# Kernel tuning notes

Measured on AMD Instinct MI355X. Metric: run time of the kernel, lower is better.

Reference implementation:

```python
import jax, jax.numpy as jnp
import numpy as np

B, N, ENC, DEC, E, ATT, V, T = 64, 196, 2048, 512, 512, 512, 32000, 32


def setup_inputs() -> dict:
    key = jax.random.key(0)
    ks = jax.random.split(key, 12)
    s = 0.02  # param init scale
    f = lambda k, shape: jax.random.normal(k, shape, jnp.float32) * s
    return {
        "features": jax.random.normal(ks[0], (B, N, ENC), jnp.float32),
        "captions": jax.random.randint(ks[1], (B, T), 0, V),
        "emb": f(ks[2], (V, E)),
        "att_Wenc": f(ks[3], (ENC, ATT)),
        "att_Wdec": f(ks[4], (DEC, ATT)),
        "att_v": f(ks[5], (ATT,)),
        "init_h_W": f(ks[6], (ENC, DEC)), "init_h_b": jnp.zeros((DEC,), jnp.float32),
        "init_c_W": f(ks[7], (ENC, DEC)), "init_c_b": jnp.zeros((DEC,), jnp.float32),
        "W_ih": f(ks[8], (4 * DEC, E + ENC)), "W_hh": f(ks[9], (4 * DEC, DEC)),
        "b_ih": jnp.zeros((4 * DEC,), jnp.float32), "b_hh": jnp.zeros((4 * DEC,), jnp.float32),
        "out_W": f(ks[10], (DEC, V)), "out_b": jnp.zeros((V,), jnp.float32),
    }


def reference(features, captions, emb, att_Wenc, att_Wdec, att_v,
              init_h_W, init_h_b, init_c_W, init_c_b,
              W_ih, W_hh, b_ih, b_hh, out_W, out_b):
    # init hidden/cell from mean-pooled encoder features
    mean_f = features.mean(axis=1)                      # [B, ENC]
    h = mean_f @ init_h_W + init_h_b                    # [B, DEC]
    c = mean_f @ init_c_W + init_c_b                    # [B, DEC]

    enc_att = features @ att_Wenc                       # [B, N, ATT] (loop-invariant)
    embs = emb[captions]                                # [B, T, E]
    xs = jnp.swapaxes(embs[:, :-1], 0, 1)               # [T-1, B, E] time-major

    def step(carry, x):
        h, c = carry
        # Bahdanau attention: tanh(Wf + Wh) . v -> softmax over spatial locations
        e = jnp.tanh(enc_att + (h @ att_Wdec)[:, None, :]) @ att_v   # [B, N]
        alpha = jax.nn.softmax(e, axis=1)                            # [B, N]
        context = jnp.einsum('bn,bnd->bd', alpha, features)          # [B, ENC]
        lstm_in = jnp.concatenate([x, context], axis=1)              # [B, E+ENC]
        gates = lstm_in @ W_ih.T + b_ih + h @ W_hh.T + b_hh          # [B, 4*DEC]
        i, f, g, o = jnp.split(gates, 4, axis=1)                     # torch gate order
        c = jax.nn.sigmoid(f) * c + jax.nn.sigmoid(i) * jnp.tanh(g)
        h = jax.nn.sigmoid(o) * jnp.tanh(c)
        out = h @ out_W + out_b                                      # dropout = identity (eval)
        return (h, c), (out, alpha)

    _, (preds, alphas) = jax.lax.scan(step, (h, c), xs)
    # back to batch-major: preds [B, T-1, V], alphas [B, T-1, N]
    return jnp.swapaxes(preds, 0, 1), jnp.swapaxes(alphas, 0, 1)
```

## Files before the change

kernel.cpp:

```cpp
#include <hip/hip_runtime.h>
#include <math.h>

constexpr int kB = 64, kN = 196, kENC = 2048, kDEC = 512, kE = 512, kATT = 512;
constexpr int kV = 32000, kT = 32, kTS = 31;
constexpr int kKIH = kE + kENC;
constexpr int kKG  = kENC + kDEC;
constexpr int kG   = 4 * kDEC;
constexpr int kSPL = 8, kKSP = kKG / kSPL;
constexpr int kM   = kTS * kB;
constexpr int kMP  = 2048;

typedef __attribute__((ext_vector_type(8))) short bf8;
typedef __attribute__((ext_vector_type(4))) float f4;
typedef __attribute__((ext_vector_type(4))) unsigned u4;

__device__ __forceinline__ f4 mfma16(bf8 a, bf8 b, f4 c){
  asm("v_mfma_f32_16x16x32_bf16 %0, %1, %2, %0" : "+v"(c) : "v"(a), "v"(b));
  return c;
}
__device__ __forceinline__ float bf2f(unsigned short u){
  return __uint_as_float(((unsigned)u) << 16);
}
__device__ __forceinline__ unsigned short f2b(float f){
  unsigned u = __float_as_uint(f);
  u += 0x7fffu + ((u >> 16) & 1u);
  return (unsigned short)(u >> 16);
}
__device__ __forceinline__ float th_(float x){
  float e2 = __expf(2.f * x);
  return 1.f - 2.f * __builtin_amdgcn_rcpf(e2 + 1.f);
}
__device__ __forceinline__ float sg_(float x){
  return __builtin_amdgcn_rcpf(1.f + __expf(-x));
}

__global__ void k_cvt(const float* __restrict__ src, unsigned short* __restrict__ dst, int n8){
  int i = blockIdx.x * 256 + threadIdx.x;
  if (i >= n8) return;
  float4 a = ((const float4*)src)[2 * i];
  float4 b = ((const float4*)src)[2 * i + 1];
  union { unsigned short u[8]; uint4 v; } t;
  t.u[0] = f2b(a.x); t.u[1] = f2b(a.y); t.u[2] = f2b(a.z); t.u[3] = f2b(a.w);
  t.u[4] = f2b(b.x); t.u[5] = f2b(b.y); t.u[6] = f2b(b.z); t.u[7] = f2b(b.w);
  ((uint4*)dst)[i] = t.v;
}

__global__ __launch_bounds__(256) void k_tcvt(const float* __restrict__ src,
                                              unsigned short* __restrict__ dst, int R, int C){
  __shared__ float t[32][33];
  int c0 = blockIdx.x * 32, r0 = blockIdx.y * 32;
  int tx = threadIdx.x & 31, ty = threadIdx.x >> 5;
  #pragma unroll
  for (int j = 0; j < 4; j++)
    t[ty + 8*j][tx] = src[(size_t)(r0 + ty + 8*j) * C + c0 + tx];
  __syncthreads();
  #pragma unroll
  for (int j = 0; j < 4; j++)
    dst[(size_t)(c0 + ty + 8*j) * R + r0 + tx] = f2b(t[tx][ty + 8*j]);
}

__global__ __launch_bounds__(256) void k_tf32(const float* __restrict__ src,
                                              float* __restrict__ dst, int R, int C){
  __shared__ float t[32][33];
  int c0 = blockIdx.x * 32, r0 = blockIdx.y * 32;
  int tx = threadIdx.x & 31, ty = threadIdx.x >> 5;
  #pragma unroll
  for (int j = 0; j < 4; j++)
    t[ty + 8*j][tx] = src[(size_t)(r0 + ty + 8*j) * C + c0 + tx];
  __syncthreads();
  #pragma unroll
  for (int j = 0; j < 4; j++)
    dst[(size_t)(c0 + ty + 8*j) * R + r0 + tx] = t[tx][ty + 8*j];
}

__global__ void k_mean(const float* __restrict__ feat, float* __restrict__ meanf){
  int b = blockIdx.x, d = blockIdx.y * 256 + threadIdx.x;
  const float* p = feat + (size_t)b * kN * kENC + d;
  float s = 0.f;
  for (int n = 0; n < kN; n++) s += p[(size_t)n * kENC];
  meanf[b * kENC + d] = s * (1.f / kN);
}

__global__ __launch_bounds__(512) void k_init(const float* __restrict__ meanf,
                       const float* __restrict__ Wh, const float* __restrict__ bh,
                       const float* __restrict__ Wc, const float* __restrict__ bc,
                       float* __restrict__ h, float* __restrict__ c){
  __shared__ float mf[kENC];
  int b = blockIdx.x;
  for (int i = threadIdx.x; i < kENC; i += 512) mf[i] = meanf[b * kENC + i];
  __syncthreads();
  int j = threadIdx.x;
  const float* W  = blockIdx.y ? Wc : Wh;
  const float* bb = blockIdx.y ? bc : bh;
  float acc = bb[j];
  for (int k = 0; k < kENC; k++) acc = fmaf(mf[k], W[k * kDEC + j], acc);
  (blockIdx.y ? c : h)[b * kDEC + j] = acc;
}

__global__ __launch_bounds__(512) void k_gather(const float* __restrict__ emb,
        const int* __restrict__ captions, unsigned short* __restrict__ Xemb){
  int m = blockIdx.x;
  int t = m >> 6, b = m & 63, d = threadIdx.x;
  Xemb[(size_t)m * kE + d] = f2b(emb[(size_t)captions[b * kT + t] * kE + d]);
}

template<int K, int LDA, int LDB, int LDC>
__global__ __launch_bounds__(256) void k_gemm_nt(const unsigned short* __restrict__ A,
                                                 const unsigned short* __restrict__ Bt,
                                                 unsigned short* __restrict__ Cb){
  int w = threadIdx.x >> 6, lane = threadIdx.x & 63;
  int m0 = blockIdx.x * 64 + w * 16, n0 = blockIdx.y * 64;
  int lr = lane & 15, lk = (lane >> 4) * 8;
  f4 acc[4] = {};
  const unsigned short* Ap = A  + (size_t)(m0 + lr) * LDA + lk;
  const unsigned short* Bp = Bt + (size_t)(n0 + lr) * LDB + lk;
  #pragma unroll 4
  for (int k0 = 0; k0 < K; k0 += 32){
    bf8 a  = *(const bf8*)(Ap + k0);
    bf8 b0 = *(const bf8*)(Bp + k0);
    bf8 b1 = *(const bf8*)(Bp + (size_t)16 * LDB + k0);
    bf8 b2 = *(const bf8*)(Bp + (size_t)32 * LDB + k0);
    bf8 b3 = *(const bf8*)(Bp + (size_t)48 * LDB + k0);
    acc[0] = mfma16(a, b0, acc[0]); acc[1] = mfma16(a, b1, acc[1]);
    acc[2] = mfma16(a, b2, acc[2]); acc[3] = mfma16(a, b3, acc[3]);
  }
  asm volatile("s_nop 7\n\ts_nop 7");
  int orow = (lane >> 4) * 4;
  #pragma unroll
  for (int nt = 0; nt < 4; nt++)
    #pragma unroll
    for (int r = 0; r < 4; r++)
      Cb[(size_t)(m0 + orow + r) * LDC + n0 + nt*16 + lr] = f2b(acc[nt][r]);
}

__global__ __launch_bounds__(256) void k_e(const unsigned short* __restrict__ EA,
                   const float* __restrict__ hWdec,
                   const float* __restrict__ attv, float* __restrict__ e){
  int w = threadIdx.x >> 6, lane = threadIdx.x & 63;
  int r = blockIdx.x * 4 + w;
  int b = r / kN;
  u4 ev = *(const u4*)(EA + (size_t)r * kATT + lane * 8);
  const float* hp = hWdec + b * kATT + lane * 8;
  const float* ap = attv + lane * 8;
  float4 h0 = *(const float4*)hp, h1 = *(const float4*)(hp + 4);
  float4 v0 = *(const float4*)ap, v1 = *(const float4*)(ap + 4);
  float s = 0.f;
  s = fmaf(th_(bf2f((unsigned short)(ev.x & 0xffffu)) + h0.x), v0.x, s);
  s = fmaf(th_(bf2f((unsigned short)(ev.x >> 16))     + h0.y), v0.y, s);
  s = fmaf(th_(bf2f((unsigned short)(ev.y & 0xffffu)) + h0.z), v0.z, s);
  s = fmaf(th_(bf2f((unsigned short)(ev.y >> 16))     + h0.w), v0.w, s);
  s = fmaf(th_(bf2f((unsigned short)(ev.z & 0xffffu)) + h1.x), v1.x, s);
  s = fmaf(th_(bf2f((unsigned short)(ev.z >> 16))     + h1.y), v1.y, s);
  s = fmaf(th_(bf2f((unsigned short)(ev.w & 0xffffu)) + h1.z), v1.z, s);
  s = fmaf(th_(bf2f((unsigned short)(ev.w >> 16))     + h1.w), v1.w, s);
  #pragma unroll
  for (int off = 32; off; off >>= 1) s += __shfl_xor(s, off, 64);
  if (lane == 0) e[r] = s;
}

__global__ __launch_bounds__(256) void k_ctx(const float* __restrict__ e,
                     const unsigned short* __restrict__ featb,
                     unsigned short* __restrict__ Xb, float* __restrict__ alphas, int t){
  __shared__ float al[kN];
  __shared__ float red[256];
  __shared__ float cred[4][64][8];
  int b = blockIdx.x, q = blockIdx.y, tid = threadIdx.x;
  float ev = (tid < kN) ? e[b * kN + tid] : -1e30f;
  red[tid] = ev; __syncthreads();
  for (int off = 128; off; off >>= 1){ if (tid < off) red[tid] = fmaxf(red[tid], red[tid + off]); __syncthreads(); }
  float mx = red[0]; __syncthreads();
  float ex = (tid < kN) ? __expf(ev - mx) : 0.f;
  red[tid] = ex; __syncthreads();
  for (int off = 128; off; off >>= 1){ if (tid < off) red[tid] += red[tid + off]; __syncthreads(); }
  float inv = 1.f / red[0];
  if (tid < kN){
    float a = ex * inv;
    al[tid] = a;
    if (q == 0) alphas[((size_t)b * kTS + t) * kN + tid] = a;
  }
  __syncthreads();
  int g = tid & 63, nq = tid >> 6;
  int d0 = q * 512 + g * 8;
  const unsigned short* fp = featb + (size_t)b * kN * kENC + d0;
  float c[8] = {0.f,0.f,0.f,0.f,0.f,0.f,0.f,0.f};
  int nbeg = nq * 49, nend = nbeg + 49;
  #pragma unroll 7
  for (int n = nbeg; n < nend; ++n){
    u4 v = *(const u4*)(fp + (size_t)n * kENC);
    float a = al[n];
    c[0] = fmaf(bf2f((unsigned short)(v.x & 0xffffu)), a, c[0]);
    c[1] = fmaf(bf2f((unsigned short)(v.x >> 16)),     a, c[1]);
    c[2] = fmaf(bf2f((unsigned short)(v.y & 0xffffu)), a, c[2]);
    c[3] = fmaf(bf2f((unsigned short)(v.y >> 16)),     a, c[3]);
    c[4] = fmaf(bf2f((unsigned short)(v.z & 0xffffu)), a, c[4]);
    c[5] = fmaf(bf2f((unsigned short)(v.z >> 16)),     a, c[5]);
    c[6] = fmaf(bf2f((unsigned short)(v.w & 0xffffu)), a, c[6]);
    c[7] = fmaf(bf2f((unsigned short)(v.w >> 16)),     a, c[7]);
  }
  if (nq){
    #pragma unroll
    for (int j = 0; j < 8; j++) cred[nq][g][j] = c[j];
  }
  __syncthreads();
  if (nq == 0){
    unsigned outw[4];
    #pragma unroll
    for (int j = 0; j < 4; j++){
      float lo = c[2*j]   + cred[1][g][2*j]   + cred[2][g][2*j]   + cred[3][g][2*j];
      float hi = c[2*j+1] + cred[1][g][2*j+1] + cred[2][g][2*j+1] + cred[3][g][2*j+1];
      outw[j] = ((unsigned)f2b(hi) << 16) | (unsigned)f2b(lo);
    }
    *(u4*)(Xb + (size_t)b * kKG + d0) = *(u4*)outw;
  }
}

__global__ __launch_bounds__(256) void k_gates(const unsigned short* __restrict__ X,
        const unsigned short* __restrict__ Wih, const unsigned short* __restrict__ Whh,
        float* __restrict__ gpart){
  int w = threadIdx.x >> 6, lane = threadIdx.x & 63;
  int n0 = blockIdx.x * 64 + w * 16, ks = blockIdx.y;
  int lr = lane & 15, lk = (lane >> 4) * 8;
  int nrow = n0 + lr;
  f4 acc[4] = {};
  const unsigned short* Xp = X + (size_t)lr * kKG + ks * kKSP + lk;
  #pragma unroll 2
  for (int kt = 0; kt < kKSP; kt += 32){
    int kk = ks * kKSP + kt + lk;
    bf8 a0 = *(const bf8*)(Xp + kt);
    bf8 a1 = *(const bf8*)(Xp + 16 * kKG + kt);
    bf8 a2 = *(const bf8*)(Xp + 32 * kKG + kt);
    bf8 a3 = *(const bf8*)(Xp + 48 * kKG + kt);
    const unsigned short* bp = (kk < kENC) ? (Wih + (size_t)nrow * kKIH + kE + kk)
                                           : (Whh + (size_t)nrow * kDEC + (kk - kENC));
    bf8 b = *(const bf8*)bp;
    acc[0] = mfma16(a0, b, acc[0]); acc[1] = mfma16(a1, b, acc[1]);
    acc[2] = mfma16(a2, b, acc[2]); acc[3] = mfma16(a3, b, acc[3]);
  }
  asm volatile("s_nop 7\n\ts_nop 7");
  float* gp = gpart + (size_t)ks * kB * kG;
  int orow = (lane >> 4) * 4;
  #pragma unroll
  for (int mt = 0; mt < 4; mt++)
    #pragma unroll
    for (int r = 0; r < 4; r++)
      gp[(size_t)(mt*16 + orow + r) * kG + n0 + lr] = acc[mt][r];
}

__global__ __launch_bounds__(512) void k_lstm(const float* __restrict__ gpart,
      const unsigned short* __restrict__ Gxb,
      const float* __restrict__ bih, const float* __restrict__ bhh,
      float* __restrict__ c, unsigned short* __restrict__ Xb,
      unsigned short* __restrict__ Hall,
      const float* __restrict__ WdecT, float* __restrict__ hWdec, int t){
  __shared__ float hl[kDEC];
  int b = blockIdx.x, d = threadIdx.x;
  int m = t * kB + b;
  float gi = 0.f, gf = 0.f, gg = 0.f, go = 0.f;
  for (int ks = 0; ks < kSPL; ks++){
    const float* gp = gpart + ((size_t)ks * kB + b) * kG;
    gi += gp[d]; gf += gp[kDEC + d]; gg += gp[2*kDEC + d]; go += gp[3*kDEC + d];
  }
  const unsigned short* gx = Gxb + (size_t)m * kG;
  gi += bf2f(gx[d])          + bih[d]          + bhh[d];
  gf += bf2f(gx[kDEC + d])   + bih[kDEC + d]   + bhh[kDEC + d];
  gg += bf2f(gx[2*kDEC + d]) + bih[2*kDEC + d] + bhh[2*kDEC + d];
  go += bf2f(gx[3*kDEC + d]) + bih[3*kDEC + d] + bhh[3*kDEC + d];
  float cn = sg_(gf) * c[b*kDEC + d] + sg_(gi) * th_(gg);
  float hn = sg_(go) * th_(cn);
  c[b*kDEC + d] = cn;
  hl[d] = hn;
  unsigned short hb = f2b(hn);
  Xb[(size_t)b*kKG + kENC + d] = hb;
  Hall[((size_t)b*kTS + t)*kDEC + d] = hb;
  __syncthreads();
  const float* wr = WdecT + (size_t)d * kATT;
  float a = 0.f;
  #pragma unroll 8
  for (int kk = 0; kk < kATT; kk += 4){
    float4 wv = *(const float4*)(wr + kk);
    a = fmaf(wv.x, hl[kk + 0], a);
    a = fmaf(wv.y, hl[kk + 1], a);
    a = fmaf(wv.z, hl[kk + 2], a);
    a = fmaf(wv.w, hl[kk + 3], a);
  }
  hWdec[b * kATT + d] = a;
}

__global__ __launch_bounds__(512) void k_prep(const float* __restrict__ h0,
      unsigned short* __restrict__ Xb,
      const float* __restrict__ WdecT, float* __restrict__ hWdec){
  __shared__ float hl[kDEC];
  int b = blockIdx.x, d = threadIdx.x;
  float hv = h0[b*kDEC + d];
  hl[d] = hv;
  Xb[(size_t)b*kKG + kENC + d] = f2b(hv);
  __syncthreads();
  const float* wr = WdecT + (size_t)d * kATT;
  float a = 0.f;
  #pragma unroll 8
  for (int kk = 0; kk < kATT; kk += 4){
    float4 wv = *(const float4*)(wr + kk);
    a = fmaf(wv.x, hl[kk + 0], a);
    a = fmaf(wv.y, hl[kk + 1], a);
    a = fmaf(wv.z, hl[kk + 2], a);
    a = fmaf(wv.w, hl[kk + 3], a);
  }
  hWdec[b * kATT + d] = a;
}

__global__ __launch_bounds__(512) void k_bigout(const unsigned short* __restrict__ Hall,
        const unsigned short* __restrict__ Wt,
        const float* __restrict__ bias, float* __restrict__ preds){
  __shared__ float st[64][128];
  int w = threadIdx.x >> 6, lane = threadIdx.x & 63;
  int n0 = blockIdx.x * 128, m0 = blockIdx.y * 256;
  int lr = lane & 15, lk = (lane >> 4) * 8;
  f4 acc[2][8];
  #pragma unroll
  for (int nt = 0; nt < 8; nt++){
    float bv = bias[n0 + nt*16 + lr];
    acc[0][nt] = (f4){bv, bv, bv, bv};
    acc[1][nt] = (f4){bv, bv, bv, bv};
  }
  const unsigned short* Ap = Hall + (size_t)(m0 + w*32 + lr) * kDEC + lk;
  const unsigned short* Bp = Wt + (size_t)(n0 + lr) * kDEC + lk;
  #pragma unroll 2
  for (int k0 = 0; k0 < kDEC; k0 += 32){
    bf8 a0 = *(const bf8*)(Ap + k0);
    bf8 a1 = *(const bf8*)(Ap + 16*kDEC + k0);
    #pragma unroll
    for (int nt = 0; nt < 8; nt++){
      bf8 b = *(const bf8*)(Bp + (size_t)nt*16*kDEC + k0);
      acc[0][nt] = mfma16(a0, b, acc[0][nt]);
      acc[1][nt] = mfma16(a1, b, acc[1][nt]);
    }
  }
  asm volatile("s_nop 7\n\ts_nop 7");
  int orow = (lane >> 4) * 4;
  for (int c = 0; c < 4; c++){
    __syncthreads();
    if ((w >> 1) == c){
      int rbase = (w & 1) * 32;
      #pragma unroll
      for (int half = 0; half < 2; half++)
        #pragma unroll
        for (int nt = 0; nt < 8; nt++)
          #pragma unroll
          for (int r = 0; r < 4; r++)
            st[rbase + half*16 + orow + r][nt*16 + lr] = acc[half][nt][r];
    }
    __syncthreads();
    int mbase = m0 + c*64;
    #pragma unroll
    for (int p = 0; p < 4; p++){
      int idx = threadIdx.x + p*512;
      int row = idx >> 5, c4 = idx & 31;
      int m = mbase + row;
      if (m < kM){
        float4 v = *(const float4*)(&st[row][c4*4]);
        *(float4*)(preds + (size_t)m * kV + n0 + c4*4) = v;
      }
    }
  }
}

extern "C" void kernel_launch(void* const* d_in, const int* in_sizes, int n_in,
                              void* d_out, int out_size, void* d_ws, size_t ws_size,
                              hipStream_t stream) {
  const float* feat     = (const float*)d_in[0];
  const int*   captions = (const int*)  d_in[1];
  const float* emb      = (const float*)d_in[2];
  const float* attWenc  = (const float*)d_in[3];
  const float* attWdec  = (const float*)d_in[4];
  const float* attv     = (const float*)d_in[5];
  const float* ihW      = (const float*)d_in[6];
  const float* ihb      = (const float*)d_in[7];
  const float* icW      = (const float*)d_in[8];
  const float* icb      = (const float*)d_in[9];
  const float* Wih      = (const float*)d_in[10];
  const float* Whh      = (const float*)d_in[11];
  const float* bih      = (const float*)d_in[12];
  const float* bhh      = (const float*)d_in[13];
  const float* outW     = (const float*)d_in[14];
  const float* outb     = (const float*)d_in[15];

  float* preds  = (float*)d_out;
  float* alphas = preds + (size_t)kB * kTS * kV;

  char* p = (char*)d_ws;
  unsigned short* featb  = (unsigned short*)p; p += (size_t)kB*kN*kENC*2;
  unsigned short* outWb  = (unsigned short*)p; p += (size_t)kV*kDEC*2;
  unsigned short* Wihb   = (unsigned short*)p; p += (size_t)kG*kKIH*2;
  unsigned short* Whhb   = (unsigned short*)p; p += (size_t)kG*kDEC*2;
  unsigned short* attWT  = (unsigned short*)p; p += (size_t)kATT*kENC*2;
  unsigned short* encattb= (unsigned short*)p; p += (size_t)kB*kN*kATT*2;
  unsigned short* Gxb    = (unsigned short*)p; p += (size_t)kMP*kG*2;
  unsigned short* Hall   = (unsigned short*)p; p += (size_t)kMP*kDEC*2;
  unsigned short* Xemb   = Hall;
  unsigned short* Xb     = (unsigned short*)p; p += (size_t)kB*kKG*2;
  float* WdecTf = (float*)p; p += (size_t)kATT*kDEC*4;
  float* gpart  = (float*)p; p += (size_t)kSPL*kB*kG*4;
  float* meanf  = (float*)p; p += (size_t)kB*kENC*4;
  float* hbuf   = (float*)p; p += (size_t)kB*kDEC*4;
  float* cws    = (float*)p; p += (size_t)kB*kDEC*4;
  float* hWdec  = (float*)p; p += (size_t)kB*kATT*4;
  float* evec   = (float*)p; p += (size_t)kB*kN*4;

  k_cvt<<<(kB*kN*kENC/8 + 255)/256, 256, 0, stream>>>(feat, featb, kB*kN*kENC/8);
  k_cvt<<<(kG*kKIH/8 + 255)/256, 256, 0, stream>>>(Wih, Wihb, kG*kKIH/8);
  k_cvt<<<(kG*kDEC/8 + 255)/256, 256, 0, stream>>>(Whh, Whhb, kG*kDEC/8);
  k_tcvt<<<dim3(kATT/32, kENC/32), 256, 0, stream>>>(attWenc, attWT, kENC, kATT);
  k_tf32<<<dim3(kATT/32, kDEC/32), 256, 0, stream>>>(attWdec, WdecTf, kDEC, kATT);
  k_tcvt<<<dim3(kV/32, kDEC/32), 256, 0, stream>>>(outW, outWb, kDEC, kV);

  k_mean<<<dim3(kB, kENC/256), 256, 0, stream>>>(feat, meanf);
  k_init<<<dim3(kB, 2), 512, 0, stream>>>(meanf, ihW, ihb, icW, icb, hbuf, cws);

  k_gather<<<kM, 512, 0, stream>>>(emb, captions, Xemb);
  k_gemm_nt<kE, kE, kKIH, kG><<<dim3(kMP/64, kG/64), 256, 0, stream>>>(Xemb, Wihb, Gxb);

  k_gemm_nt<kENC, kENC, kENC, kATT><<<dim3(kB*kN/64, kATT/64), 256, 0, stream>>>(featb, attWT, encattb);

  k_prep<<<kB, 512, 0, stream>>>(hbuf, Xb, WdecTf, hWdec);

  for (int t = 0; t < kTS; ++t) {
    k_e<<<kB*kN/4, 256, 0, stream>>>(encattb, hWdec, attv, evec);
    k_ctx<<<dim3(kB, 4), 256, 0, stream>>>(evec, featb, Xb, alphas, t);
    k_gates<<<dim3(kG/64, kSPL), 256, 0, stream>>>(Xb, Wihb, Whhb, gpart);
    k_lstm<<<kB, 512, 0, stream>>>(gpart, Gxb, bih, bhh, cws, Xb, Hall,
                                   WdecTf, hWdec, t);
  }

  k_bigout<<<dim3(kV/128, kMP/256), 512, 0, stream>>>(Hall, outWb, outb, preds);
}
```

Measured before the change: 2.521 ms.

## Fuse feature conversion with mean, fuse gates GEMM with LSTM cell, retile encoder GEMM

Merges the bf16 conversion of features with the spatial mean so the large feature tensor is read once. Inside the recurrent loop, replaces the split-K gates GEMM plus a separate LSTM kernel with one kernel that computes all four gates for a 16-column slice and applies the cell update directly. This removes the partial-sum buffer, but the fused kernel uses only 32 blocks. The attention projection GEMM is reordered with N-tiles on the fast grid axis and nontemporal A loads, and the bigout shared-memory tile is padded to reduce bank conflicts.

```diff
diff --git a/kernel.cpp b/kernel.cpp
--- a/kernel.cpp
+++ b/kernel.cpp
@@ -6,7 +6,6 @@
 constexpr int kKIH = kE + kENC;
 constexpr int kKG  = kENC + kDEC;
 constexpr int kG   = 4 * kDEC;
-constexpr int kSPL = 8, kKSP = kKG / kSPL;
 constexpr int kM   = kTS * kB;
 constexpr int kMP  = 2048;
 
@@ -45,6 +44,30 @@
   ((uint4*)dst)[i] = t.v;
 }
 
+__global__ __launch_bounds__(256) void k_cvtmean(const float* __restrict__ feat,
+        unsigned short* __restrict__ featb, float* __restrict__ meanp){
+  int b = blockIdx.x, nq = blockIdx.y, tid = threadIdx.x;
+  int d0 = tid * 8;
+  const float* fp = feat + (size_t)b * kN * kENC + d0;
+  unsigned short* op = featb + (size_t)b * kN * kENC + d0;
+  float s[8] = {0.f,0.f,0.f,0.f,0.f,0.f,0.f,0.f};
+  int nbeg = nq * 49, nend = nbeg + 49;
+  #pragma unroll 4
+  for (int n = nbeg; n < nend; ++n){
+    float4 a = *(const float4*)(fp + (size_t)n * kENC);
+    float4 c = *(const float4*)(fp + (size_t)n * kENC + 4);
+    union { unsigned short u[8]; u4 v; } t;
+    t.u[0] = f2b(a.x); t.u[1] = f2b(a.y); t.u[2] = f2b(a.z); t.u[3] = f2b(a.w);
+    t.u[4] = f2b(c.x); t.u[5] = f2b(c.y); t.u[6] = f2b(c.z); t.u[7] = f2b(c.w);
+    *(u4*)(op + (size_t)n * kENC) = t.v;
+    s[0] += a.x; s[1] += a.y; s[2] += a.z; s[3] += a.w;
+    s[4] += c.x; s[5] += c.y; s[6] += c.z; s[7] += c.w;
+  }
+  float* mp = meanp + ((size_t)b * 4 + nq) * kENC + d0;
+  #pragma unroll
+  for (int j = 0; j < 8; j++) mp[j] = s[j];
+}
+
 __global__ __launch_bounds__(256) void k_tcvt(const float* __restrict__ src,
                                               unsigned short* __restrict__ dst, int R, int C){
   __shared__ float t[32][33];
@@ -73,21 +96,15 @@
     dst[(size_t)(c0 + ty + 8*j) * R + r0 + tx] = t[tx][ty + 8*j];
 }
 
-__global__ void k_mean(const float* __restrict__ feat, float* __restrict__ meanf){
-  int b = blockIdx.x, d = blockIdx.y * 256 + threadIdx.x;
-  const float* p = feat + (size_t)b * kN * kENC + d;
-  float s = 0.f;
-  for (int n = 0; n < kN; n++) s += p[(size_t)n * kENC];
-  meanf[b * kENC + d] = s * (1.f / kN);
-}
-
-__global__ __launch_bounds__(512) void k_init(const float* __restrict__ meanf,
+__global__ __launch_bounds__(512) void k_init(const float* __restrict__ meanp,
                        const float* __restrict__ Wh, const float* __restrict__ bh,
                        const float* __restrict__ Wc, const float* __restrict__ bc,
                        float* __restrict__ h, float* __restrict__ c){
   __shared__ float mf[kENC];
   int b = blockIdx.x;
-  for (int i = threadIdx.x; i < kENC; i += 512) mf[i] = meanf[b * kENC + i];
+  const float* mp = meanp + (size_t)b * 4 * kENC;
+  for (int i = threadIdx.x; i < kENC; i += 512)
+    mf[i] = (mp[i] + mp[kENC + i] + mp[2*kENC + i] + mp[3*kENC + i]) * (1.f / kN);
   __syncthreads();
   int j = threadIdx.x;
   const float* W  = blockIdx.y ? Wc : Wh;
@@ -131,6 +148,35 @@
     #pragma unroll
     for (int r = 0; r < 4; r++)
       Cb[(size_t)(m0 + orow + r) * LDC + n0 + nt*16 + lr] = f2b(acc[nt][r]);
+}
+
+__global__ __launch_bounds__(256) void k_encatt2(const unsigned short* __restrict__ A,
+                                                 const unsigned short* __restrict__ Bt,
+                                                 unsigned short* __restrict__ Cb){
+  int w = threadIdx.x >> 6, lane = threadIdx.x & 63;
+  int n0 = blockIdx.x * 64;
+  int m0 = blockIdx.y * 64 + w * 16;
+  int lr = lane & 15, lk = (lane >> 4) * 8;
+  f4 acc[4] = {};
+  const unsigned short* Ap = A  + (size_t)(m0 + lr) * kENC + lk;
+  const unsigned short* Bp = Bt + (size_t)(n0 + lr) * kENC + lk;
+  #pragma unroll 8
+  for (int k0 = 0; k0 < kENC; k0 += 32){
+    bf8 a  = __builtin_nontemporal_load((const bf8*)(Ap + k0));
+    bf8 b0 = *(const bf8*)(Bp + k0);
+    bf8 b1 = *(const bf8*)(Bp + (size_t)16 * kENC + k0);
+    bf8 b2 = *(const bf8*)(Bp + (size_t)32 * kENC + k0);
+    bf8 b3 = *(const bf8*)(Bp + (size_t)48 * kENC + k0);
+    acc[0] = mfma16(a, b0, acc[0]); acc[1] = mfma16(a, b1, acc[1]);
+    acc[2] = mfma16(a, b2, acc[2]); acc[3] = mfma16(a, b3, acc[3]);
+  }
+  asm volatile("s_nop 7\n\ts_nop 7");
+  int orow = (lane >> 4) * 4;
+  #pragma unroll
+  for (int nt = 0; nt < 4; nt++)
+    #pragma unroll
+    for (int r = 0; r < 4; r++)
+      Cb[(size_t)(m0 + orow + r) * kATT + n0 + nt*16 + lr] = f2b(acc[nt][r]);
 }
 
 __global__ __launch_bounds__(256) void k_e(const unsigned short* __restrict__ EA,
@@ -214,64 +260,84 @@
   }
 }
 
-__global__ __launch_bounds__(256) void k_gates(const unsigned short* __restrict__ X,
-        const unsigned short* __restrict__ Wih, const unsigned short* __restrict__ Whh,
-        float* __restrict__ gpart){
-  int w = threadIdx.x >> 6, lane = threadIdx.x & 63;
-  int n0 = blockIdx.x * 64 + w * 16, ks = blockIdx.y;
-  int lr = lane & 15, lk = (lane >> 4) * 8;
-  int nrow = n0 + lr;
-  f4 acc[4] = {};
-  const unsigned short* Xp = X + (size_t)lr * kKG + ks * kKSP + lk;
-  #pragma unroll 2
-  for (int kt = 0; kt < kKSP; kt += 32){
-    int kk = ks * kKSP + kt + lk;
-    bf8 a0 = *(const bf8*)(Xp + kt);
-    bf8 a1 = *(const bf8*)(Xp + 16 * kKG + kt);
-    bf8 a2 = *(const bf8*)(Xp + 32 * kKG + kt);
-    bf8 a3 = *(const bf8*)(Xp + 48 * kKG + kt);
-    const unsigned short* bp = (kk < kENC) ? (Wih + (size_t)nrow * kKIH + kE + kk)
-                                           : (Whh + (size_t)nrow * kDEC + (kk - kENC));
-    bf8 b = *(const bf8*)bp;
-    acc[0] = mfma16(a0, b, acc[0]); acc[1] = mfma16(a1, b, acc[1]);
-    acc[2] = mfma16(a2, b, acc[2]); acc[3] = mfma16(a3, b, acc[3]);
-  }
-  asm volatile("s_nop 7\n\ts_nop 7");
-  float* gp = gpart + (size_t)ks * kB * kG;
-  int orow = (lane >> 4) * 4;
-  #pragma unroll
-  for (int mt = 0; mt < 4; mt++)
-    #pragma unroll
-    for (int r = 0; r < 4; r++)
-      gp[(size_t)(mt*16 + orow + r) * kG + n0 + lr] = acc[mt][r];
-}
-
-__global__ __launch_bounds__(512) void k_lstm(const float* __restrict__ gpart,
+__global__ __launch_bounds__(512) void k_gl(const unsigned short* __restrict__ Xb,
+      const unsigned short* __restrict__ Wihb, const unsigned short* __restrict__ Whhb,
       const unsigned short* __restrict__ Gxb,
       const float* __restrict__ bih, const float* __restrict__ bhh,
-      float* __restrict__ c, unsigned short* __restrict__ Xb,
-      unsigned short* __restrict__ Hall,
-      const float* __restrict__ WdecT, float* __restrict__ hWdec, int t){
+      float* __restrict__ cws, float* __restrict__ hbuf,
+      unsigned short* __restrict__ XbMut, unsigned short* __restrict__ Hall, int t){
+  __shared__ float gex[4][2][16][16];
+  int blk = blockIdx.x, tid = threadIdx.x;
+  int w = tid >> 6, lane = tid & 63;
+  int d0 = blk * 16;
+  int mt = w & 3;
+  int gp = (w >> 2) * 2;
+  int lr = lane & 15, lk = (lane >> 4) * 8;
+  f4 acc0 = {0.f,0.f,0.f,0.f}, acc1 = {0.f,0.f,0.f,0.f};
+  int g0row = (gp    )*kDEC + d0 + lr;
+  int g1row = (gp + 1)*kDEC + d0 + lr;
+  const unsigned short* Xp = Xb + (size_t)(mt*16 + lr)*kKG + lk;
+  const unsigned short* B0 = Wihb + (size_t)g0row*kKIH + kE + lk;
+  const unsigned short* B1 = Wihb + (size_t)g1row*kKIH + kE + lk;
+  #pragma unroll 4
+  for (int kt = 0; kt < kENC; kt += 32){
+    bf8 a  = *(const bf8*)(Xp + kt);
+    bf8 b0 = *(const bf8*)(B0 + kt);
+    bf8 b1 = *(const bf8*)(B1 + kt);
+    acc0 = mfma16(a, b0, acc0);
+    acc1 = mfma16(a, b1, acc1);
+  }
+  const unsigned short* Xh = Xb + (size_t)(mt*16 + lr)*kKG + kENC + lk;
+  const unsigned short* H0 = Whhb + (size_t)g0row*kDEC + lk;
+  const unsigned short* H1 = Whhb + (size_t)g1row*kDEC + lk;
+  #pragma unroll 4
+  for (int kt = 0; kt < kDEC; kt += 32){
+    bf8 a  = *(const bf8*)(Xh + kt);
+    bf8 b0 = *(const bf8*)(H0 + kt);
+    bf8 b1 = *(const bf8*)(H1 + kt);
+    acc0 = mfma16(a, b0, acc0);
+    acc1 = mfma16(a, b1, acc1);
+  }
+  asm volatile("s_nop 7\n\ts_nop 7");
+  int orow = (lane >> 4) * 4;
+  if (w >= 4){
+    #pragma unroll
+    for (int r = 0; r < 4; r++){
+      gex[mt][0][orow + r][lr] = acc0[r];
+      gex[mt][1][orow + r][lr] = acc1[r];
+    }
+  }
+  __syncthreads();
+  if (w < 4){
+    int d = d0 + lr;
+    float bi_i = bih[d]          + bhh[d];
+    float bi_f = bih[kDEC + d]   + bhh[kDEC + d];
+    float bi_g = bih[2*kDEC + d] + bhh[2*kDEC + d];
+    float bi_o = bih[3*kDEC + d] + bhh[3*kDEC + d];
+    #pragma unroll
+    for (int r = 0; r < 4; r++){
+      int b = mt*16 + orow + r;
+      const unsigned short* gx = Gxb + (size_t)(t*kB + b) * kG;
+      float gi = acc0[r]                + bf2f(gx[d])          + bi_i;
+      float gf = acc1[r]                + bf2f(gx[kDEC + d])   + bi_f;
+      float gg = gex[mt][0][orow+r][lr] + bf2f(gx[2*kDEC + d]) + bi_g;
+      float go = gex[mt][1][orow+r][lr] + bf2f(gx[3*kDEC + d]) + bi_o;
+      float cn = sg_(gf) * cws[b*kDEC + d] + sg_(gi) * th_(gg);
+      float hn = sg_(go) * th_(cn);
+      cws[b*kDEC + d]  = cn;
+      hbuf[b*kDEC + d] = hn;
+      unsigned short hb = f2b(hn);
+      XbMut[(size_t)b*kKG + kENC + d] = hb;
+      Hall[((size_t)b*kTS + t)*kDEC + d] = hb;
+    }
+  }
+}
+
+__global__ __launch_bounds__(512) void k_hwdec(const float* __restrict__ hbuf,
+      const float* __restrict__ WdecT, float* __restrict__ hWdec){
   __shared__ float hl[kDEC];
   int b = blockIdx.x, d = threadIdx.x;
-  int m = t * kB + b;
-  float gi = 0.f, gf = 0.f, gg = 0.f, go = 0.f;
-  for (int ks = 0; ks < kSPL; ks++){
-    const float* gp = gpart + ((size_t)ks * kB + b) * kG;
-    gi += gp[d]; gf += gp[kDEC + d]; gg += gp[2*kDEC + d]; go += gp[3*kDEC + d];
-  }
-  const unsigned short* gx = Gxb + (size_t)m * kG;
-  gi += bf2f(gx[d])          + bih[d]          + bhh[d];
-  gf += bf2f(gx[kDEC + d])   + bih[kDEC + d]   + bhh[kDEC + d];
-  gg += bf2f(gx[2*kDEC + d]) + bih[2*kDEC + d] + bhh[2*kDEC + d];
-  go += bf2f(gx[3*kDEC + d]) + bih[3*kDEC + d] + bhh[3*kDEC + d];
-  float cn = sg_(gf) * c[b*kDEC + d] + sg_(gi) * th_(gg);
-  float hn = sg_(go) * th_(cn);
-  c[b*kDEC + d] = cn;
-  hl[d] = hn;
-  unsigned short hb = f2b(hn);
-  Xb[(size_t)b*kKG + kENC + d] = hb;
-  Hall[((size_t)b*kTS + t)*kDEC + d] = hb;
+  hl[d] = hbuf[b*kDEC + d];
   __syncthreads();
   const float* wr = WdecT + (size_t)d * kATT;
   float a = 0.f;
@@ -308,10 +374,11 @@
   hWdec[b * kATT + d] = a;
 }
 
+constexpr int kLDW = 132;
 __global__ __launch_bounds__(512) void k_bigout(const unsigned short* __restrict__ Hall,
         const unsigned short* __restrict__ Wt,
         const float* __restrict__ bias, float* __restrict__ preds){
-  __shared__ float st[64][128];
+  __shared__ float st[64][kLDW];
   int w = threadIdx.x >> 6, lane = threadIdx.x & 63;
   int n0 = blockIdx.x * 128, m0 = blockIdx.y * 256;
   int lr = lane & 15, lk = (lane >> 4) * 8;
@@ -399,36 +466,34 @@
   unsigned short* Xemb   = Hall;
   unsigned short* Xb     = (unsigned short*)p; p += (size_t)kB*kKG*2;
   float* WdecTf = (float*)p; p += (size_t)kATT*kDEC*4;
-  float* gpart  = (float*)p; p += (size_t)kSPL*kB*kG*4;
-  float* meanf  = (float*)p; p += (size_t)kB*kENC*4;
+  float* meanp  = (float*)p; p += (size_t)kB*4*kENC*4;
   float* hbuf   = (float*)p; p += (size_t)kB*kDEC*4;
   float* cws    = (float*)p; p += (size_t)kB*kDEC*4;
   float* hWdec  = (float*)p; p += (size_t)kB*kATT*4;
   float* evec   = (float*)p; p += (size_t)kB*kN*4;
 
-  k_cvt<<<(kB*kN*kENC/8 + 255)/256, 256, 0, stream>>>(feat, featb, kB*kN*kENC/8);
+  k_cvtmean<<<dim3(kB, 4), 256, 0, stream>>>(feat, featb, meanp);
   k_cvt<<<(kG*kKIH/8 + 255)/256, 256, 0, stream>>>(Wih, Wihb, kG*kKIH/8);
   k_cvt<<<(kG*kDEC/8 + 255)/256, 256, 0, stream>>>(Whh, Whhb, kG*kDEC/8);
   k_tcvt<<<dim3(kATT/32, kENC/32), 256, 0, stream>>>(attWenc, attWT, kENC, kATT);
   k_tf32<<<dim3(kATT/32, kDEC/32), 256, 0, stream>>>(attWdec, WdecTf, kDEC, kATT);
   k_tcvt<<<dim3(kV/32, kDEC/32), 256, 0, stream>>>(outW, outWb, kDEC, kV);
 
-  k_mean<<<dim3(kB, kENC/256), 256, 0, stream>>>(feat, meanf);
-  k_init<<<dim3(kB, 2), 512, 0, stream>>>(meanf, ihW, ihb, icW, icb, hbuf, cws);
+  k_init<<<dim3(kB, 2), 512, 0, stream>>>(meanp, ihW, ihb, icW, icb, hbuf, cws);
 
   k_gather<<<kM, 512, 0, stream>>>(emb, captions, Xemb);
   k_gemm_nt<kE, kE, kKIH, kG><<<dim3(kMP/64, kG/64), 256, 0, stream>>>(Xemb, Wihb, Gxb);
 
-  k_gemm_nt<kENC, kENC, kENC, kATT><<<dim3(kB*kN/64, kATT/64), 256, 0, stream>>>(featb, attWT, encattb);
+  k_encatt2<<<dim3(kATT/64, kB*kN/64), 256, 0, stream>>>(featb, attWT, encattb);
 
   k_prep<<<kB, 512, 0, stream>>>(hbuf, Xb, WdecTf, hWdec);
 
   for (int t = 0; t < kTS; ++t) {
     k_e<<<kB*kN/4, 256, 0, stream>>>(encattb, hWdec, attv, evec);
     k_ctx<<<dim3(kB, 4), 256, 0, stream>>>(evec, featb, Xb, alphas, t);
-    k_gates<<<dim3(kG/64, kSPL), 256, 0, stream>>>(Xb, Wihb, Whhb, gpart);
-    k_lstm<<<kB, 512, 0, stream>>>(gpart, Gxb, bih, bhh, cws, Xb, Hall,
-                                   WdecTf, hWdec, t);
+    k_gl<<<32, 512, 0, stream>>>(Xb, Wihb, Whhb, Gxb, bih, bhh, cws, hbuf,
+                                 Xb, Hall, t);
+    k_hwdec<<<kB, 512, 0, stream>>>(hbuf, WdecTf, hWdec);
   }
 
   k_bigout<<<dim3(kV/128, kMP/256), 512, 0, stream>>>(Hall, outWb, outb, preds);
```

Result: slower. 3.930 ms (+55.8%).
